# Performance work log

Hardware: AMD Instinct MI355X
Metric: run time of the kernel (lower is better)

## Reference

```python
import jax, jax.numpy as jnp
import numpy as np

N_SRC, N_TGT, E = 50000, 50000, 1600000
SRC_IN, TGT_IN, H, L = 64, 64, 128, 3
N = N_SRC + N_TGT


def setup_inputs() -> dict:
    key = jax.random.key(0)
    ks = jax.random.split(key, 12)
    s = 1.0 / np.sqrt(H)
    return {
        "src_x": jax.random.normal(ks[0], (N_SRC, SRC_IN), jnp.float32),
        "tgt_x": jax.random.normal(ks[1], (N_TGT, TGT_IN), jnp.float32),
        "edge_index": jax.random.randint(ks[2], (2, E), 0, N, jnp.int32),
        "Wsrc": jax.random.normal(ks[3], (H, SRC_IN), jnp.float32) / np.sqrt(SRC_IN),
        "bsrc": jnp.zeros((H,), jnp.float32),
        "Wtgt": jax.random.normal(ks[4], (H, TGT_IN), jnp.float32) / np.sqrt(TGT_IN),
        "btgt": jnp.zeros((H,), jnp.float32),
        "Wl": jax.random.normal(ks[5], (L, H, H), jnp.float32) * s,  # neighbor-aggregate weight
        "bl": jnp.zeros((L, H), jnp.float32),
        "Wr": jax.random.normal(ks[6], (L, H, H), jnp.float32) * s,  # root (self) weight, no bias
    }


def reference(src_x, tgt_x, edge_index, Wsrc, bsrc, Wtgt, btgt, Wl, bl, Wr):
    src_idx, dst_idx = edge_index[0], edge_index[1]
    # input projections + concat over node dim
    x = jnp.concatenate([src_x @ Wsrc.T + bsrc, tgt_x @ Wtgt.T + btgt], axis=0)  # [N,H]
    # in-degree for mean aggregation (computed once; edge structure is fixed)
    deg = jax.ops.segment_sum(jnp.ones((E,), x.dtype), dst_idx, num_segments=N)
    inv_deg = (1.0 / jnp.maximum(deg, 1.0))[:, None]  # [N,1]
    h = x
    for i in range(L):
        msg = h[src_idx]  # gather: [E,H]
        agg = jax.ops.segment_sum(msg, dst_idx, num_segments=N) * inv_deg  # mean aggr
        # PyG SAGEConv: lin_l(mean_neighbors) + lin_r(self); lin_l has bias
        h = agg @ Wl[i].T + bl[i] + h @ Wr[i].T
        if i + 1 < L:
            h = jax.nn.relu(h)  # dropout p=0.0 (eval) -> identity
    return h
```

## Files before the change

kernel.cpp:

```cpp
#include <hip/hip_runtime.h>
#include <hip/hip_fp8.h>

#define NSRC 50000
#define NTGT 50000
#define NTOT 100000
#define NE   1600000
#define IND  64
#define HD   128
#define CAP  64
#define CHUNK2 2048
#define NCH2 782
#define SBIN 128
#define NBIN 782
#define PROJB 391
#define PACKB 48

typedef short s16x8 __attribute__((ext_vector_type(8)));
typedef float f32x4 __attribute__((ext_vector_type(4)));

__device__ __forceinline__ ushort f2bf(float f) {
  union { float f; uint u; } v; v.f = f;
  const uint r = v.u + 0x7fffu + ((v.u >> 16) & 1u);
  return (ushort)(r >> 16);
}
__device__ __forceinline__ float bfl(uint v) {
  union { uint u; float f; } c; c.u = v << 16; return c.f;
}
__device__ __forceinline__ float bfh(uint v) {
  union { uint u; float f; } c; c.u = v & 0xffff0000u; return c.f;
}

__device__ void pack_dev(const float* __restrict__ Wl, const float* __restrict__ Wr,
                         ushort* __restrict__ wpk, const int bid) {
  const int idx = bid * 256 + threadIdx.x;
  const int layer = idx >> 12;
  const int r = idx & 4095;
  const int which = r >> 11;
  const int g = r & 2047;
  const int cf = g >> 8;
  const int t = (g >> 6) & 3;
  const int lane = g & 63;
  const int lr = lane & 15;
  const int kc = (lane >> 4) * 8;
  const float* W = (which ? Wr : Wl) + (size_t)layer * HD * HD;
  const float* src = W + (size_t)(cf * 16 + lr) * HD + t * 32 + kc;
  const float4 a = *(const float4*)(src);
  const float4 b = *(const float4*)(src + 4);
  s16x8 o;
  o[0] = (short)f2bf(a.x); o[1] = (short)f2bf(a.y);
  o[2] = (short)f2bf(a.z); o[3] = (short)f2bf(a.w);
  o[4] = (short)f2bf(b.x); o[5] = (short)f2bf(b.y);
  o[6] = (short)f2bf(b.z); o[7] = (short)f2bf(b.w);
  *(s16x8*)(wpk + (size_t)idx * 8) = o;
}

__device__ void proj_dev(const float* __restrict__ x, const float* __restrict__ W,
                         const float* __restrict__ b, ushort* __restrict__ out,
                         const int count, const int out_base, const int bid) {
  const int lane = threadIdx.x & 63;
  const int wave = threadIdx.x >> 6;
  const int n0 = bid * 128 + wave * 32;
  const int lr = lane & 15;
  const int kc = (lane >> 4) * 8;
  const int rowq = (lane >> 4) * 4;

  s16x8 af[2][2];
#pragma unroll
  for (int r = 0; r < 2; ++r) {
    int ar = n0 + 16 * r + lr;
    if (ar >= count) ar = count - 1;
#pragma unroll
    for (int t = 0; t < 2; ++t) {
      const float* xp = x + (size_t)ar * IND + t * 32 + kc;
      const float4 xa = *(const float4*)(xp);
      const float4 xb = *(const float4*)(xp + 4);
      s16x8 a;
      a[0] = (short)f2bf(xa.x); a[1] = (short)f2bf(xa.y);
      a[2] = (short)f2bf(xa.z); a[3] = (short)f2bf(xa.w);
      a[4] = (short)f2bf(xb.x); a[5] = (short)f2bf(xb.y);
      a[6] = (short)f2bf(xb.z); a[7] = (short)f2bf(xb.w);
      af[r][t] = a;
    }
  }
#pragma unroll
  for (int cf = 0; cf < 8; ++cf) {
    const float* wp = W + (size_t)(cf * 16 + lr) * IND + kc;
    s16x8 w0, w1;
    {
      const float4 wa = *(const float4*)(wp);
      const float4 wb = *(const float4*)(wp + 4);
      const float4 wc = *(const float4*)(wp + 32);
      const float4 wd = *(const float4*)(wp + 36);
      w0[0] = (short)f2bf(wa.x); w0[1] = (short)f2bf(wa.y);
      w0[2] = (short)f2bf(wa.z); w0[3] = (short)f2bf(wa.w);
      w0[4] = (short)f2bf(wb.x); w0[5] = (short)f2bf(wb.y);
      w0[6] = (short)f2bf(wb.z); w0[7] = (short)f2bf(wb.w);
      w1[0] = (short)f2bf(wc.x); w1[1] = (short)f2bf(wc.y);
      w1[2] = (short)f2bf(wc.z); w1[3] = (short)f2bf(wc.w);
      w1[4] = (short)f2bf(wd.x); w1[5] = (short)f2bf(wd.y);
      w1[6] = (short)f2bf(wd.z); w1[7] = (short)f2bf(wd.w);
    }
    f32x4 acc0 = {0.f, 0.f, 0.f, 0.f};
    f32x4 acc1 = {0.f, 0.f, 0.f, 0.f};
    acc0 = __builtin_amdgcn_mfma_f32_16x16x32_bf16(af[0][0], w0, acc0, 0, 0, 0);
    acc1 = __builtin_amdgcn_mfma_f32_16x16x32_bf16(af[1][0], w0, acc1, 0, 0, 0);
    acc0 = __builtin_amdgcn_mfma_f32_16x16x32_bf16(af[0][1], w1, acc0, 0, 0, 0);
    acc1 = __builtin_amdgcn_mfma_f32_16x16x32_bf16(af[1][1], w1, acc1, 0, 0, 0);
    const int col = cf * 16 + lr;
    const float bv = b[col];
#pragma unroll
    for (int r = 0; r < 2; ++r) {
      const f32x4 acc = r ? acc1 : acc0;
#pragma unroll
      for (int q = 0; q < 4; ++q) {
        const int row = n0 + 16 * r + rowq + q;
        if (row < count) out[(size_t)(out_base + row) * HD + col] = f2bf(acc[q] + bv);
      }
    }
  }
}

__device__ void part2a_dev(const int* __restrict__ dst, uint* __restrict__ bincnt, const int bid) {
  __shared__ uint hist[NBIN];
  const int tid = threadIdx.x;
  const int i0 = bid * CHUNK2;
  const int i1 = (i0 + CHUNK2 < NE) ? i0 + CHUNK2 : NE;
  for (int j = tid; j < NBIN; j += 256) hist[j] = 0;
  __syncthreads();
  for (int i = i0 + tid; i < i1; i += 256)
    atomicAdd(&hist[((uint)dst[i]) >> 7], 1u);
  __syncthreads();
  for (int j = tid; j < NBIN; j += 256)
    if (hist[j]) atomicAdd(&bincnt[j], hist[j]);
}

__global__ __launch_bounds__(256) void prep_kernel(
    const float* __restrict__ src_x, const float* __restrict__ tgt_x,
    const float* __restrict__ Wsrc, const float* __restrict__ bsrc,
    const float* __restrict__ Wtgt, const float* __restrict__ btgt,
    ushort* __restrict__ hbuf,
    const int* __restrict__ dst, uint* __restrict__ bincnt,
    const float* __restrict__ Wl, const float* __restrict__ Wr,
    ushort* __restrict__ wpk) {
  const int b = blockIdx.x;
  if (b < PROJB) {
    proj_dev(src_x, Wsrc, bsrc, hbuf, NSRC, 0, b);
  } else if (b < 2 * PROJB) {
    proj_dev(tgt_x, Wtgt, btgt, hbuf, NTGT, NSRC, b - PROJB);
  } else if (b < 2 * PROJB + NCH2) {
    part2a_dev(dst, bincnt, b - 2 * PROJB);
  } else {
    pack_dev(Wl, Wr, wpk, b - 2 * PROJB - NCH2);
  }
}

__global__ __launch_bounds__(256) void scan_kernel(const uint* __restrict__ bincnt,
                                                   uint* __restrict__ binoff, uint* __restrict__ bincur) {
  __shared__ uint lds[256];
  const int tid = threadIdx.x;
  uint v[4]; uint s = 0;
#pragma unroll
  for (int j = 0; j < 4; ++j) {
    const int idx = tid * 4 + j;
    v[j] = (idx < NBIN) ? bincnt[idx] : 0;
    s += v[j];
  }
  lds[tid] = s;
  __syncthreads();
  for (int off = 1; off < 256; off <<= 1) {
    const uint t = (tid >= off) ? lds[tid - off] : 0;
    __syncthreads();
    lds[tid] += t;
    __syncthreads();
  }
  uint run = lds[tid] - s;
#pragma unroll
  for (int j = 0; j < 4; ++j) {
    const int idx = tid * 4 + j;
    if (idx < NBIN) { binoff[idx] = run; bincur[idx] = run; }
    else if (idx == NBIN) binoff[idx] = run;
    run += v[j];
  }
}

__global__ __launch_bounds__(256) void part2b_kernel(const int* __restrict__ src, const int* __restrict__ dst,
                                                     uint* __restrict__ bincur, uint* __restrict__ ebuf2) {
  __shared__ uint hist[NBIN];
  __shared__ uint base[NBIN];
  const int tid = threadIdx.x;
  const int i0 = blockIdx.x * CHUNK2;
  const int i1 = (i0 + CHUNK2 < NE) ? i0 + CHUNK2 : NE;
  for (int j = tid; j < NBIN; j += 256) hist[j] = 0;
  __syncthreads();
  for (int i = i0 + tid; i < i1; i += 256)
    atomicAdd(&hist[((uint)dst[i]) >> 7], 1u);
  __syncthreads();
  for (int j = tid; j < NBIN; j += 256) {
    if (hist[j]) base[j] = atomicAdd(&bincur[j], hist[j]);
    hist[j] = 0;
  }
  __syncthreads();
  for (int i = i0 + tid; i < i1; i += 256) {
    const uint d = (uint)dst[i];
    const uint bin = d >> 7;
    const uint pos = base[bin] + atomicAdd(&hist[bin], 1u);
    ebuf2[pos] = (uint)src[i] | ((d & 127u) << 17);
  }
}

__global__ __launch_bounds__(256) void part3_kernel(const uint* __restrict__ binoff, const uint* __restrict__ ebuf2,
                                                    uint* __restrict__ csr, int* __restrict__ rowstart) {
  __shared__ uint slotL[SBIN][CAP];
  __shared__ uint cntL[SBIN];
  __shared__ uint scanL[SBIN];
  const int tid = threadIdx.x;
  const int b = blockIdx.x;
  const int e0 = (int)binoff[b];
  const int e1 = (int)binoff[b + 1];
  for (int j = tid; j < SBIN; j += 256) cntL[j] = 0;
  __syncthreads();
  for (int i = e0 + tid; i < e1; i += 256) {
    const uint rec = ebuf2[i];
    const uint dl = rec >> 17;
    const uint pos = atomicAdd(&cntL[dl], 1u);
    if (pos < CAP) slotL[dl][pos] = rec & 0x1FFFFu;
  }
  __syncthreads();
  if (tid < SBIN) {
    uint cv = cntL[tid];
    scanL[tid] = cv < CAP ? cv : CAP;
  }
  __syncthreads();
  for (int off = 1; off < SBIN; off <<= 1) {
    uint t = 0;
    if (tid < SBIN && tid >= off) t = scanL[tid - off];
    __syncthreads();
    if (tid < SBIN) scanL[tid] += t;
    __syncthreads();
  }
  if (tid < SBIN) {
    const int node = b * SBIN + tid;
    const uint m = (cntL[tid] < CAP) ? cntL[tid] : CAP;
    const uint myoff = (uint)e0 + scanL[tid] - m;
    if (node < NTOT) {
      rowstart[node] = (int)myoff;
      for (uint j = 0; j < m; ++j) csr[myoff + j] = slotL[tid][j];
    }
  }
  if (b == NBIN - 1 && tid == 0) rowstart[NTOT] = e0 + (int)scanL[SBIN - 1];
}

__global__ __launch_bounds__(256) void cvt8_kernel(const ushort* __restrict__ h, uchar* __restrict__ h8) {
  const size_t idx = (size_t)blockIdx.x * 256 + threadIdx.x;
  const uint4 v = ((const uint4*)h)[idx];
  __hip_fp8x2_e4m3 q0(make_float2(bfl(v.x), bfh(v.x)));
  __hip_fp8x2_e4m3 q1(make_float2(bfl(v.y), bfh(v.y)));
  __hip_fp8x2_e4m3 q2(make_float2(bfl(v.z), bfh(v.z)));
  __hip_fp8x2_e4m3 q3(make_float2(bfl(v.w), bfh(v.w)));
  uint2 o;
  o.x = (uint)q0.__x | ((uint)q1.__x << 16);
  o.y = (uint)q2.__x | ((uint)q3.__x << 16);
  ((uint2*)h8)[idx] = o;
}

__global__ __launch_bounds__(256) void agg4_kernel(const uchar* __restrict__ h8, ushort* __restrict__ agg,
                                                   const int* __restrict__ rowstart, const uint* __restrict__ csr) {
  const int g = threadIdx.x >> 4;
  const int l16 = threadIdx.x & 15;
  const int n = blockIdx.x * 16 + g;
  const int r0 = rowstart[n];
  const int r1 = rowstart[n + 1];
  const uint2* hp = (const uint2*)h8;
  float a0 = 0.f, a1 = 0.f, a2 = 0.f, a3 = 0.f, a4 = 0.f, a5 = 0.f, a6 = 0.f, a7 = 0.f;
  __hip_fp8x2_e4m3 p;
#define ACC8(w) { \
    p.__x = (__hip_fp8x2_storage_t)((w).x & 0xFFFFu); { float2 f = (float2)p; a0 += f.x; a1 += f.y; } \
    p.__x = (__hip_fp8x2_storage_t)((w).x >> 16);     { float2 f = (float2)p; a2 += f.x; a3 += f.y; } \
    p.__x = (__hip_fp8x2_storage_t)((w).y & 0xFFFFu); { float2 f = (float2)p; a4 += f.x; a5 += f.y; } \
    p.__x = (__hip_fp8x2_storage_t)((w).y >> 16);     { float2 f = (float2)p; a6 += f.x; a7 += f.y; } }
  int i = r0;
  for (; i + 8 <= r1; i += 8) {
    uint s[8];
    uint2 v[8];
#pragma unroll
    for (int u = 0; u < 8; ++u) s[u] = csr[i + u];
#pragma unroll
    for (int u = 0; u < 8; ++u) v[u] = hp[(size_t)s[u] * 16 + l16];
#pragma unroll
    for (int u = 0; u < 8; ++u) ACC8(v[u]);
  }
  for (; i + 4 <= r1; i += 4) {
    uint s[4];
    uint2 v[4];
#pragma unroll
    for (int u = 0; u < 4; ++u) s[u] = csr[i + u];
#pragma unroll
    for (int u = 0; u < 4; ++u) v[u] = hp[(size_t)s[u] * 16 + l16];
#pragma unroll
    for (int u = 0; u < 4; ++u) ACC8(v[u]);
  }
  for (; i < r1; ++i) {
    const uint2 v = hp[(size_t)csr[i] * 16 + l16];
    ACC8(v);
  }
#undef ACC8
  const int deg = r1 - r0;
  const float sc = 1.0f / (float)(deg > 1 ? deg : 1);
  uint4 o;
  o.x = (uint)f2bf(a0 * sc) | ((uint)f2bf(a1 * sc) << 16);
  o.y = (uint)f2bf(a2 * sc) | ((uint)f2bf(a3 * sc) << 16);
  o.z = (uint)f2bf(a4 * sc) | ((uint)f2bf(a5 * sc) << 16);
  o.w = (uint)f2bf(a6 * sc) | ((uint)f2bf(a7 * sc) << 16);
  ((uint4*)agg)[(size_t)n * 16 + l16] = o;
}

__global__ __launch_bounds__(256) void mfma_gemm_kernel(
    const ushort* A, const ushort* Hm,
    const ushort* __restrict__ Wlp, const float* __restrict__ bl,
    const ushort* __restrict__ Wrp, void* outv, uchar* __restrict__ h8out,
    const int relu, const int f32out) {
  __shared__ ushort res[128][136];
  const int lane = threadIdx.x & 63;
  const int wave = threadIdx.x >> 6;
  const int n0 = blockIdx.x * 128;
  const int wrow = wave * 32;
  const int lr = lane & 15;
  const int kc = (lane >> 4) * 8;
  const int rowq = (lane >> 4) * 4;

  s16x8 af[2][4], hf[2][4];
#pragma unroll
  for (int r = 0; r < 2; ++r) {
    int ar = n0 + wrow + 16 * r + lr;
    if (ar >= NTOT) ar = NTOT - 1;
    const ushort* ap = A + (size_t)ar * HD + kc;
    const ushort* hp = Hm + (size_t)ar * HD + kc;
#pragma unroll
    for (int t = 0; t < 4; ++t) {
      af[r][t] = *(const s16x8*)(ap + t * 32);
      hf[r][t] = *(const s16x8*)(hp + t * 32);
    }
  }

  s16x8 wl[4], wr[4], wln[4], wrn[4];
#pragma unroll
  for (int t = 0; t < 4; ++t) {
    wl[t] = *(const s16x8*)(Wlp + (size_t)(t * 64 + lane) * 8);
    wr[t] = *(const s16x8*)(Wrp + (size_t)(t * 64 + lane) * 8);
  }
#pragma unroll
  for (int cf = 0; cf < 8; ++cf) {
    if (cf < 7) {
#pragma unroll
      for (int t = 0; t < 4; ++t) {
        wln[t] = *(const s16x8*)(Wlp + (size_t)(((cf + 1) * 4 + t) * 64 + lane) * 8);
        wrn[t] = *(const s16x8*)(Wrp + (size_t)(((cf + 1) * 4 + t) * 64 + lane) * 8);
      }
    }
    f32x4 acc0 = {0.f, 0.f, 0.f, 0.f};
    f32x4 acc1 = {0.f, 0.f, 0.f, 0.f};
#pragma unroll
    for (int t = 0; t < 4; ++t) {
      acc0 = __builtin_amdgcn_mfma_f32_16x16x32_bf16(af[0][t], wl[t], acc0, 0, 0, 0);
      acc1 = __builtin_amdgcn_mfma_f32_16x16x32_bf16(af[1][t], wl[t], acc1, 0, 0, 0);
      acc0 = __builtin_amdgcn_mfma_f32_16x16x32_bf16(hf[0][t], wr[t], acc0, 0, 0, 0);
      acc1 = __builtin_amdgcn_mfma_f32_16x16x32_bf16(hf[1][t], wr[t], acc1, 0, 0, 0);
    }
    const float bv = bl[cf * 16 + lr];
    const int col = cf * 16 + lr;
#pragma unroll
    for (int r = 0; r < 2; ++r) {
      const f32x4 acc = r ? acc1 : acc0;
#pragma unroll
      for (int q = 0; q < 4; ++q) {
        float v = acc[q] + bv;
        if (relu && v < 0.f) v = 0.f;
        res[wrow + 16 * r + rowq + q][col] = f2bf(v);
      }
    }
#pragma unroll
    for (int t = 0; t < 4; ++t) { wl[t] = wln[t]; wr[t] = wrn[t]; }
  }
  __syncthreads();
  const int tid = threadIdx.x;
#pragma unroll
  for (int k = 0; k < 8; ++k) {
    const int idx = k * 256 + tid;
    const int r = idx >> 4;
    const int c = idx & 15;
    const int grow = n0 + r;
    if (grow < NTOT) {
      const uint4 v = *(const uint4*)&res[r][c * 8];
      if (f32out) {
        float4 f0 = make_float4(bfl(v.x), bfh(v.x), bfl(v.y), bfh(v.y));
        float4 f1 = make_float4(bfl(v.z), bfh(v.z), bfl(v.w), bfh(v.w));
        ((float4*)outv)[(size_t)grow * 32 + c * 2] = f0;
        ((float4*)outv)[(size_t)grow * 32 + c * 2 + 1] = f1;
      } else {
        ((uint4*)outv)[(size_t)grow * 16 + c] = v;
        __hip_fp8x2_e4m3 q0(make_float2(bfl(v.x), bfh(v.x)));
        __hip_fp8x2_e4m3 q1(make_float2(bfl(v.y), bfh(v.y)));
        __hip_fp8x2_e4m3 q2(make_float2(bfl(v.z), bfh(v.z)));
        __hip_fp8x2_e4m3 q3(make_float2(bfl(v.w), bfh(v.w)));
        uint2 o;
        o.x = (uint)q0.__x | ((uint)q1.__x << 16);
        o.y = (uint)q2.__x | ((uint)q3.__x << 16);
        ((uint2*)h8out)[(size_t)grow * 16 + c] = o;
      }
    }
  }
}

extern "C" void kernel_launch(void* const* d_in, const int* in_sizes, int n_in,
                              void* d_out, int out_size, void* d_ws, size_t ws_size,
                              hipStream_t stream) {
  const float* src_x = (const float*)d_in[0];
  const float* tgt_x = (const float*)d_in[1];
  const int*   eidx  = (const int*)d_in[2];
  const float* Wsrc  = (const float*)d_in[3];
  const float* bsrc  = (const float*)d_in[4];
  const float* Wtgt  = (const float*)d_in[5];
  const float* btgt  = (const float*)d_in[6];
  const float* Wl    = (const float*)d_in[7];
  const float* bl    = (const float*)d_in[8];
  const float* Wr    = (const float*)d_in[9];
  float* out = (float*)d_out;
  (void)in_sizes; (void)n_in; (void)out_size; (void)ws_size;

  char* ws = (char*)d_ws;
  size_t off = 0;
  auto alloc = [&](size_t bytes) -> void* {
    void* p = (void*)(ws + off);
    off = (off + bytes + 511) & ~(size_t)511;
    return p;
  };
  ushort* hbuf   = (ushort*)alloc((size_t)NTOT * HD * sizeof(ushort));
  ushort* abuf   = (ushort*)alloc((size_t)NTOT * HD * sizeof(ushort));
  ushort* wpk    = (ushort*)alloc((size_t)3 * 2 * 2048 * 8 * sizeof(ushort));
  uint*   bincnt = (uint*)alloc(NBIN * sizeof(uint));
  uint*   binoff = (uint*)alloc((NBIN + 1) * sizeof(uint));
  uint*   bincur = (uint*)alloc(NBIN * sizeof(uint));

  uint*  dout_u   = (uint*)d_out;
  uint*  ebuf2    = dout_u;
  uint*  csr      = dout_u + 1700000;
  int*   rowstart = (int*)(dout_u + 3400000);
  uchar* h8buf    = (uchar*)(dout_u + 3600000);

  const int* src_idx = eidx;
  const int* dst_idx = eidx + NE;

  hipMemsetAsync(bincnt, 0, NBIN * sizeof(uint), stream);

  prep_kernel<<<2 * PROJB + NCH2 + PACKB, 256, 0, stream>>>(
      src_x, tgt_x, Wsrc, bsrc, Wtgt, btgt, hbuf, dst_idx, bincnt, Wl, Wr, wpk);

  scan_kernel<<<1, 256, 0, stream>>>(bincnt, binoff, bincur);
  part2b_kernel<<<NCH2, 256, 0, stream>>>(src_idx, dst_idx, bincur, ebuf2);
  part3_kernel<<<NBIN, 256, 0, stream>>>(binoff, ebuf2, csr, rowstart);

  const int cgrid = NTOT * HD / 8 / 256;
  const int agrid = NTOT / 16;
  const int ggrid = (NTOT + 127) / 128;
  const size_t WPL = 2048 * 8;
  cvt8_kernel<<<cgrid, 256, 0, stream>>>(hbuf, h8buf);
  agg4_kernel<<<agrid, 256, 0, stream>>>(h8buf, abuf, rowstart, csr);
  mfma_gemm_kernel<<<ggrid, 256, 0, stream>>>(abuf, hbuf, wpk, bl, wpk + WPL, abuf, h8buf, 1, 0);
  agg4_kernel<<<agrid, 256, 0, stream>>>(h8buf, hbuf, rowstart, csr);
  mfma_gemm_kernel<<<ggrid, 256, 0, stream>>>(hbuf, abuf, wpk + 2 * WPL, bl + HD, wpk + 3 * WPL, hbuf, h8buf, 1, 0);
  agg4_kernel<<<agrid, 256, 0, stream>>>(h8buf, abuf, rowstart, csr);
  mfma_gemm_kernel<<<ggrid, 256, 0, stream>>>(abuf, hbuf, wpk + 4 * WPL, bl + 2 * HD, wpk + 5 * WPL, out, h8buf, 0, 1);
}
```

Measured before the change: 280.2 us.

## Replace atomic bin cursors with per-chunk histogram matrix and column scan

```diff
diff --git a/kernel.cpp b/kernel.cpp
--- a/kernel.cpp
+++ b/kernel.cpp
@@ -9,9 +9,10 @@
 #define HD   128
 #define CAP  64
 #define CHUNK2 2048
-#define NCH2 782
+#define NCH2 784
 #define SBIN 128
 #define NBIN 782
+#define NBINP 784
 #define PROJB 391
 #define PACKB 48
 
@@ -29,6 +30,7 @@
 __device__ __forceinline__ float bfh(uint v) {
   union { uint u; float f; } c; c.u = v & 0xffff0000u; return c.f;
 }
+__device__ __forceinline__ int permj(int j) { return (j % 98) * 8 + j / 98; }
 
 __device__ void pack_dev(const float* __restrict__ Wl, const float* __restrict__ Wr,
                          ushort* __restrict__ wpk, const int bid) {
@@ -120,7 +122,8 @@
   }
 }
 
-__device__ void part2a_dev(const int* __restrict__ dst, uint* __restrict__ bincnt, const int bid) {
+__device__ void part2a_dev(const int* __restrict__ dst, uint* __restrict__ bincnt,
+                           uint* __restrict__ histmat, const int bid) {
   __shared__ uint hist[NBIN];
   const int tid = threadIdx.x;
   const int i0 = bid * CHUNK2;
@@ -130,8 +133,10 @@
   for (int i = i0 + tid; i < i1; i += 256)
     atomicAdd(&hist[((uint)dst[i]) >> 7], 1u);
   __syncthreads();
-  for (int j = tid; j < NBIN; j += 256)
+  for (int j = tid; j < NBIN; j += 256) {
+    histmat[(size_t)bid * NBIN + j] = hist[j];
     if (hist[j]) atomicAdd(&bincnt[j], hist[j]);
+  }
 }
 
 __global__ __launch_bounds__(256) void prep_kernel(
@@ -139,7 +144,7 @@
     const float* __restrict__ Wsrc, const float* __restrict__ bsrc,
     const float* __restrict__ Wtgt, const float* __restrict__ btgt,
     ushort* __restrict__ hbuf,
-    const int* __restrict__ dst, uint* __restrict__ bincnt,
+    const int* __restrict__ dst, uint* __restrict__ bincnt, uint* __restrict__ histmat,
     const float* __restrict__ Wl, const float* __restrict__ Wr,
     ushort* __restrict__ wpk) {
   const int b = blockIdx.x;
@@ -148,14 +153,14 @@
   } else if (b < 2 * PROJB) {
     proj_dev(tgt_x, Wtgt, btgt, hbuf, NTGT, NSRC, b - PROJB);
   } else if (b < 2 * PROJB + NCH2) {
-    part2a_dev(dst, bincnt, b - 2 * PROJB);
+    part2a_dev(dst, bincnt, histmat, b - 2 * PROJB);
   } else {
     pack_dev(Wl, Wr, wpk, b - 2 * PROJB - NCH2);
   }
 }
 
 __global__ __launch_bounds__(256) void scan_kernel(const uint* __restrict__ bincnt,
-                                                   uint* __restrict__ binoff, uint* __restrict__ bincur) {
+                                                   uint* __restrict__ binoff) {
   __shared__ uint lds[256];
   const int tid = threadIdx.x;
   uint v[4]; uint s = 0;
@@ -177,33 +182,64 @@
 #pragma unroll
   for (int j = 0; j < 4; ++j) {
     const int idx = tid * 4 + j;
-    if (idx < NBIN) { binoff[idx] = run; bincur[idx] = run; }
+    if (idx < NBIN) binoff[idx] = run;
     else if (idx == NBIN) binoff[idx] = run;
     run += v[j];
   }
 }
 
+__global__ __launch_bounds__(256) void colscan_kernel(const uint* __restrict__ histmat,
+                                                      const uint* __restrict__ binoff,
+                                                      uint* __restrict__ offmat) {
+  const int bin = (blockIdx.x % 8) * 98 + blockIdx.x / 8;
+  if (bin >= NBIN) return;
+  __shared__ uint h[NCH2];
+  __shared__ uint ps[256];
+  const int tid = threadIdx.x;
+  for (int j = tid; j < NCH2; j += 256)
+    h[j] = histmat[(size_t)permj(j) * NBIN + bin];
+  __syncthreads();
+  uint s = 0;
+  if (tid < 196) {
+#pragma unroll
+    for (int u = 0; u < 4; ++u) s += h[tid * 4 + u];
+  }
+  ps[tid] = s;
+  __syncthreads();
+  for (int off = 1; off < 256; off <<= 1) {
+    const uint t = (tid >= off) ? ps[tid - off] : 0;
+    __syncthreads();
+    ps[tid] += t;
+    __syncthreads();
+  }
+  if (tid < 196) {
+    uint run = binoff[bin] + ps[tid] - s;
+#pragma unroll
+    for (int u = 0; u < 4; ++u) {
+      const int j = tid * 4 + u;
+      offmat[(size_t)permj(j) * NBIN + bin] = run;
+      run += h[j];
+    }
+  }
+}
+
 __global__ __launch_bounds__(256) void part2b_kernel(const int* __restrict__ src, const int* __restrict__ dst,
-                                                     uint* __restrict__ bincur, uint* __restrict__ ebuf2) {
-  __shared__ uint hist[NBIN];
+                                                     const uint* __restrict__ offmat, uint* __restrict__ ebuf2) {
   __shared__ uint base[NBIN];
+  __shared__ uint cur[NBIN];
   const int tid = threadIdx.x;
-  const int i0 = blockIdx.x * CHUNK2;
+  const int bid = blockIdx.x;
+  for (int j = tid; j < NBIN; j += 256) {
+    base[j] = offmat[(size_t)bid * NBIN + j];
+    cur[j] = 0;
+  }
+  __syncthreads();
+  const int i0 = bid * CHUNK2;
   const int i1 = (i0 + CHUNK2 < NE) ? i0 + CHUNK2 : NE;
-  for (int j = tid; j < NBIN; j += 256) hist[j] = 0;
-  __syncthreads();
-  for (int i = i0 + tid; i < i1; i += 256)
-    atomicAdd(&hist[((uint)dst[i]) >> 7], 1u);
-  __syncthreads();
-  for (int j = tid; j < NBIN; j += 256) {
-    if (hist[j]) base[j] = atomicAdd(&bincur[j], hist[j]);
-    hist[j] = 0;
-  }
-  __syncthreads();
   for (int i = i0 + tid; i < i1; i += 256) {
     const uint d = (uint)dst[i];
     const uint bin = d >> 7;
-    const uint pos = base[bin] + atomicAdd(&hist[bin], 1u);
+    const uint pos = base[bin] + atomicAdd(&cur[bin], 1u);
     ebuf2[pos] = (uint)src[i] | ((d & 127u) << 17);
   }
 }
@@ -439,13 +475,14 @@
   ushort* wpk    = (ushort*)alloc((size_t)3 * 2 * 2048 * 8 * sizeof(ushort));
   uint*   bincnt = (uint*)alloc(NBIN * sizeof(uint));
   uint*   binoff = (uint*)alloc((NBIN + 1) * sizeof(uint));
-  uint*   bincur = (uint*)alloc(NBIN * sizeof(uint));
 
   uint*  dout_u   = (uint*)d_out;
   uint*  ebuf2    = dout_u;
   uint*  csr      = dout_u + 1700000;
   int*   rowstart = (int*)(dout_u + 3400000);
   uchar* h8buf    = (uchar*)(dout_u + 3600000);
+  uint*  histmat  = dout_u + 6900000;
+  uint*  offmat   = dout_u + 7600000;
 
   const int* src_idx = eidx;
   const int* dst_idx = eidx + NE;
@@ -453,10 +490,11 @@
   hipMemsetAsync(bincnt, 0, NBIN * sizeof(uint), stream);
 
   prep_kernel<<<2 * PROJB + NCH2 + PACKB, 256, 0, stream>>>(
-      src_x, tgt_x, Wsrc, bsrc, Wtgt, btgt, hbuf, dst_idx, bincnt, Wl, Wr, wpk);
-
-  scan_kernel<<<1, 256, 0, stream>>>(bincnt, binoff, bincur);
-  part2b_kernel<<<NCH2, 256, 0, stream>>>(src_idx, dst_idx, bincur, ebuf2);
+      src_x, tgt_x, Wsrc, bsrc, Wtgt, btgt, hbuf, dst_idx, bincnt, histmat, Wl, Wr, wpk);
+
+  scan_kernel<<<1, 256, 0, stream>>>(bincnt, binoff);
+  colscan_kernel<<<NBINP, 256, 0, stream>>>(histmat, binoff, offmat);
+  part2b_kernel<<<NCH2, 256, 0, stream>>>(src_idx, dst_idx, offmat, ebuf2);
   part3_kernel<<<NBIN, 256, 0, stream>>>(binoff, ebuf2, csr, rowstart);
 
   const int cgrid = NTOT * HD / 8 / 256;
```

New measurement: 262.3 us. 6.4% less time.
